# Kernel tuning notes

Measured on AMD Instinct MI355X. Metric: run time of the kernel, lower is better.

Reference implementation:

```python
import jax, jax.numpy as jnp
import numpy as np

B, N, H, E, OBS, A, AFF, EFF = 2, 50000, 64, 1_000_000, 128, 18, 512, 256


def setup_inputs() -> dict:
    key = jax.random.key(0)
    ks = jax.random.split(key, 20)
    s = 0.05  # small init to keep gates/tanh unsaturated
    return {
        "obs": jax.random.normal(ks[0], (B, OBS), jnp.float32),
        "state": jax.random.normal(ks[1], (B, N, H), jnp.float32) * 0.1,
        "W_in": jax.random.normal(ks[2], (OBS, H), jnp.float32) * s,
        "b_in": jnp.zeros((H,), jnp.float32),
        "W_msg": jax.random.normal(ks[3], (H, H), jnp.float32) * s,
        "W_gate": jax.random.normal(ks[4], (2 * H, H), jnp.float32) * s,
        "b_gate": jnp.zeros((H,), jnp.float32),
        "W_cand": jax.random.normal(ks[5], (2 * H, H), jnp.float32) * s,
        "b_cand": jnp.zeros((H,), jnp.float32),
        "W_dec": jax.random.normal(ks[6], (H, H), jnp.float32) * s,
        "b_dec": jnp.zeros((H,), jnp.float32),
        "W_mean": jax.random.normal(ks[7], (H, A), jnp.float32) * s,
        "b_mean": jnp.zeros((A,), jnp.float32),
        "W_ls": jax.random.normal(ks[8], (H, A), jnp.float32) * s,
        "b_ls": jnp.zeros((A,), jnp.float32),
        "src_index": jax.random.randint(ks[9], (E,), 0, N),
        "dst_index": jax.random.randint(ks[10], (E,), 0, N),
        "afferent_idx": jax.random.randint(ks[11], (AFF,), 0, N),
        "efferent_idx": jax.random.randint(ks[12], (EFF,), 0, N),
    }


def reference(obs, state, W_in, b_in, W_msg, W_gate, b_gate, W_cand, b_cand,
              W_dec, b_dec, W_mean, b_mean, W_ls, b_ls,
              src_index, dst_index, afferent_idx, efferent_idx):
    # inject obs projection into afferent node slots
    projected = obs @ W_in + b_in                                   # [B, H]
    injected = jnp.zeros_like(state).at[:, afferent_idx, :].set(projected[:, None, :])
    # gather-project-scatter message passing over the edge list
    src_msgs = state[:, src_index, :] @ W_msg                       # [B, E, H]
    messages = jnp.zeros_like(state).at[:, dst_index, :].add(src_msgs)
    # GRU-style gated update
    combined = messages + injected
    gate_in = jnp.concatenate([state, combined], axis=-1)           # [B, N, 2H]
    z = jax.nn.sigmoid(gate_in @ W_gate + b_gate)
    cand = jnp.tanh(gate_in @ W_cand + b_cand)
    next_state = (1.0 - z) * state + z * cand
    # mean-pool readout over efferent nodes, then policy heads
    readout = next_state[:, efferent_idx, :].mean(axis=1)           # [B, H]
    decoded = jnp.tanh(readout @ W_dec + b_dec)
    mean = decoded @ W_mean + b_mean
    log_std = jnp.clip(decoded @ W_ls + b_ls, -5.0, 2.0)
    return mean, log_std, next_state
```

## Files before the change

### kernel.cpp

```cpp
#include <hip/hip_runtime.h>
#include <hip/hip_bf16.h>

constexpr int kN   = 50000;
constexpr int kH   = 64;
constexpr int kB   = 2;
constexpr int kE   = 1000000;
constexpr int kObs = 128;
constexpr int kA   = 18;
constexpr int kAff = 512;
constexpr int kEff = 256;
constexpr int kNH  = kN * kH;
constexpr int kOutOff = 2 * kB * kA;
constexpr int kRanges = 8;
constexpr int kNr  = kN / kRanges;
constexpr int kChunks = 64;
constexpr int kEc  = kE / kChunks;
constexpr int kHistB = kRanges * kChunks;
constexpr int kPackPerR = (kNr + 127) / 128;
constexpr int kPackBlocks = kRanges * kPackPerR;
constexpr int kWprepBlocks = 20;
constexpr int kScanB = (kN + 255) / 256;
constexpr int kGatB = kRanges * 1563;
constexpr int kUpdPerR = (kNr + 31) / 32;
constexpr int kUpdB = kRanges * kUpdPerR;

typedef __attribute__((ext_vector_type(8))) short short8_t;
typedef __attribute__((ext_vector_type(4))) float f32x4_t;

__device__ __forceinline__ float ldf(const void* p, int i, int f32) {
  if (f32) return ((const float*)p)[i];
  unsigned short u = ((const unsigned short*)p)[i];
  union { unsigned int x; float f; } v; v.x = ((unsigned int)u) << 16; return v.f;
}
__device__ __forceinline__ void stf(void* p, int i, float val, int f32) {
  if (f32) ((float*)p)[i] = val;
  else ((__hip_bfloat16*)p)[i] = __float2bfloat16(val);
}
__device__ __forceinline__ float lo16(unsigned int w) {
  union { unsigned int i; float f; } v; v.i = w << 16; return v.f;
}
__device__ __forceinline__ float hi16(unsigned int w) {
  union { unsigned int i; float f; } v; v.i = w & 0xffff0000u; return v.f;
}
__device__ __forceinline__ float b2f(unsigned short u) {
  union { unsigned int i; float f; } v; v.i = ((unsigned int)u) << 16; return v.f;
}
__device__ __forceinline__ unsigned int f2b(float f) {
  union { float f; unsigned int u; } v; v.f = f;
  unsigned int r = v.u + 0x7fffu + ((v.u >> 16) & 1u);
  return r >> 16;
}
__device__ __forceinline__ float fsig(float x) {
  return __builtin_amdgcn_rcpf(1.f + __expf(-x));
}
__device__ __forceinline__ float ftanh(float x) {
  return 1.f - 2.f * __builtin_amdgcn_rcpf(__expf(2.f * x) + 1.f);
}
__device__ __forceinline__ int detect64(const unsigned short* wprobe, int t) {
  int hits = 0;
  for (int k = 0; k < 4; ++k) {
    unsigned short u = wprobe[(t * 4 + k) * 2];
    int e = (u >> 7) & 0xFF;
    if ((u & 0x7FFFu) != 0 && e >= 108 && e <= 128) hits++;
  }
  for (int off = 32; off; off >>= 1) hits += __shfl_down(hits, off);
  return (hits < 128) ? 1 : 0;
}

extern "C" __global__ __launch_bounds__(1024) void k_prep(
    const unsigned short* __restrict__ wprobe,
    const void* __restrict__ obs,
    const void* __restrict__ W_in,
    const void* __restrict__ b_in,
    const int* __restrict__ aff_idx,
    const int* __restrict__ dst,
    const void* __restrict__ W_msg,
    const void* __restrict__ W_gate,
    const void* __restrict__ W_cand,
    int* __restrict__ dflag,
    int* __restrict__ flags,
    float* __restrict__ projected,
    int* __restrict__ deg_c,
    unsigned short* __restrict__ wt,
    float* __restrict__ eff_acc) {
  __shared__ int sdeg[kNr];
  int t = threadIdx.x, b = blockIdx.x;
  if (b == 0) {
    __shared__ int sflag;
    if (t < 64) { int f = detect64(wprobe, t); if (t == 0) { sflag = f; dflag[0] = f; } }
    for (int i = t; i < kN; i += 1024) flags[i] = 0;
    if (t < 128) eff_acc[t] = 0.f;
    __syncthreads();
    int f32 = sflag;
    if (t < kAff) flags[aff_idx[t]] = 1;
    if (t < kB * kH) {
      int bb = t >> 6, h = t & 63;
      float acc = ldf(b_in, h, f32);
      for (int o = 0; o < kObs; ++o)
        acc += ldf(obs, bb * kObs + o, f32) * ldf(W_in, o * kH + h, f32);
      projected[t] = acc;
    }
  } else if (b <= kHistB) {
    int h = b - 1, r = h & 7, c = h >> 3;
    int r0 = r * kNr;
    for (int i = t; i < kNr; i += 1024) sdeg[i] = 0;
    __syncthreads();
    int end = (c + 1) * kEc;
    for (int e = c * kEc + t; e < end; e += 1024) {
      unsigned rel = (unsigned)(dst[e] - r0);
      if (rel < (unsigned)kNr) atomicAdd(&sdeg[rel], 1);
    }
    __syncthreads();
    for (int i = t; i < kNr; i += 1024) deg_c[c * kN + r0 + i] = sdeg[i];
  } else {
    __shared__ int sflag;
    if (t < 64) { int f = detect64(wprobe, t); if (t == 0) sflag = f; }
    __syncthreads();
    int f32 = sflag;
    int i = (b - 1 - kHistB) * 1024 + t;
    if (i < 4096) {
      int n = i >> 6, k = i & 63;
      wt[i] = (unsigned short)f2b(ldf(W_msg, k * 64 + n, f32));
    } else if (i < 12288) {
      int j = i - 4096; int n = j >> 7, k = j & 127;
      wt[i] = (unsigned short)f2b(ldf(W_gate, k * 64 + n, f32));
    } else if (i < 20480) {
      int j = i - 12288; int n = j >> 7, k = j & 127;
      wt[i] = (unsigned short)f2b(ldf(W_cand, k * 64 + n, f32));
    }
  }
}

extern "C" __global__ void k_scan1(const int* __restrict__ deg_c,
                                   int* __restrict__ row_off,
                                   int* __restrict__ partials) {
  __shared__ int sd[256];
  int t = threadIdx.x;
  int n = blockIdx.x * 256 + t;
  int s = 0;
  if (n < kN) {
    for (int c = 0; c < kChunks; ++c) s += deg_c[c * kN + n];
  }
  sd[t] = s;
  __syncthreads();
  for (int off = 1; off < 256; off <<= 1) {
    int v = (t >= off) ? sd[t - off] : 0;
    __syncthreads();
    sd[t] += v;
    __syncthreads();
  }
  int excl = sd[t] - s;
  if (t == 255) partials[blockIdx.x] = sd[255];
  if (n < kN) row_off[n] = excl;
}

extern "C" __global__ void k_scan3(int* __restrict__ row_off,
                                   const int* __restrict__ partials,
                                   int* __restrict__ deg_c) {
  __shared__ int sd[256];
  int t = threadIdx.x;
  int s = 0;
  for (int j = t; j < (int)blockIdx.x; j += 256) s += partials[j];
  sd[t] = s;
  __syncthreads();
  for (int off = 128; off; off >>= 1) {
    if (t < off) sd[t] += sd[t + off];
    __syncthreads();
  }
  int base = sd[0];
  int n = blockIdx.x * 256 + t;
  if (n < kN) {
    int v = row_off[n] + base;
    row_off[n] = v;
    int run = v;
#pragma unroll 8
    for (int c = 0; c < kChunks; ++c) {
      int d = deg_c[c * kN + n];
      deg_c[c * kN + n] = run;
      run += d;
    }
  }
  if (blockIdx.x == 0 && t == 0) row_off[kN] = kE;
}

extern "C" __global__ __launch_bounds__(1024) void k_scatter(
    const int* __restrict__ src,
    const int* __restrict__ dst,
    const int* __restrict__ chunk_base,
    int* __restrict__ sorted_src,
    const unsigned short* __restrict__ wprobe,
    const void* __restrict__ state,
    unsigned int* __restrict__ pack) {
  __shared__ int scur[kNr];
  int t = threadIdx.x;
  if (blockIdx.x < kHistB) {
    int r = blockIdx.x & 7, c = blockIdx.x >> 3;
    int r0 = r * kNr;
    for (int i = t; i < kNr; i += 1024) scur[i] = chunk_base[c * kN + r0 + i];
    __syncthreads();
    int end = (c + 1) * kEc;
    for (int e = c * kEc + t; e < end; e += 1024) {
      unsigned rel = (unsigned)(dst[e] - r0);
      if (rel < (unsigned)kNr) {
        int pos = atomicAdd(&scur[rel], 1);
        sorted_src[pos] = src[e];
      }
    }
  } else {
    __shared__ int sflag;
    if (t < 64) { int f = detect64(wprobe, t); if (t == 0) sflag = f; }
    __syncthreads();
    int f32 = sflag;
    int p = blockIdx.x - kHistB;
    int x = p & 7, j = p >> 3;
    int nb = x * kNr + j * 128;
    int nl = min(nb + 128, (x + 1) * kNr);
    int i = nb * 64 + t * 8;
    if (i < nl * 64) {
      uint4 o0, o1;
      if (!f32) {
        uint4 a = *(const uint4*)((const unsigned short*)state + i);
        uint4 c4 = *(const uint4*)((const unsigned short*)state + kNH + i);
        o0.x = (a.x & 0xffffu) | (c4.x << 16);
        o0.y = (a.x >> 16)     | (c4.x & 0xffff0000u);
        o0.z = (a.y & 0xffffu) | (c4.y << 16);
        o0.w = (a.y >> 16)     | (c4.y & 0xffff0000u);
        o1.x = (a.z & 0xffffu) | (c4.z << 16);
        o1.y = (a.z >> 16)     | (c4.z & 0xffff0000u);
        o1.z = (a.w & 0xffffu) | (c4.w << 16);
        o1.w = (a.w >> 16)     | (c4.w & 0xffff0000u);
      } else {
        const float* sf = (const float*)state;
        unsigned int w[8];
#pragma unroll
        for (int k = 0; k < 8; ++k)
          w[k] = f2b(sf[i + k]) | (f2b(sf[kNH + i + k]) << 16);
        o0 = make_uint4(w[0], w[1], w[2], w[3]);
        o1 = make_uint4(w[4], w[5], w[6], w[7]);
      }
      *(uint4*)&pack[i] = o0;
      *(uint4*)&pack[i + 4] = o1;
    }
  }
}

extern "C" __global__ __launch_bounds__(256) void k_gather(
    const unsigned int* __restrict__ pack,
    const int* __restrict__ row_off,
    const int* __restrict__ sorted_src,
    unsigned int* __restrict__ agg) {
  int wave = threadIdx.x >> 6, lane = threadIdx.x & 63;
  int x = blockIdx.x & 7, j = blockIdx.x >> 3;
  int local = j * 4 + wave;
  if (local >= kNr) return;
  int n = x * kNr + local;
  int s  = row_off[n];
  int en = row_off[n + 1];
  int g = lane >> 4, col = lane & 15;
  const uint4* pk4 = (const uint4*)pack;
  float a0x = 0.f, a0y = 0.f, a0z = 0.f, a0w = 0.f;
  float a1x = 0.f, a1y = 0.f, a1z = 0.f, a1w = 0.f;
  for (int e = s; e < en; e += 8) {
#pragma unroll
    for (int h = 0; h < 2; ++h) {
      int ee = e + h * 4 + g;
      int idx = sorted_src[min(ee, en - 1)];
      uint4 wv = pk4[idx * 16 + col];
      if (ee >= en) { wv.x = 0u; wv.y = 0u; wv.z = 0u; wv.w = 0u; }
      a0x += lo16(wv.x); a1x += hi16(wv.x);
      a0y += lo16(wv.y); a1y += hi16(wv.y);
      a0z += lo16(wv.z); a1z += hi16(wv.z);
      a0w += lo16(wv.w); a1w += hi16(wv.w);
    }
  }
  a0x += __shfl_xor(a0x, 16); a0x += __shfl_xor(a0x, 32);
  a0y += __shfl_xor(a0y, 16); a0y += __shfl_xor(a0y, 32);
  a0z += __shfl_xor(a0z, 16); a0z += __shfl_xor(a0z, 32);
  a0w += __shfl_xor(a0w, 16); a0w += __shfl_xor(a0w, 32);
  a1x += __shfl_xor(a1x, 16); a1x += __shfl_xor(a1x, 32);
  a1y += __shfl_xor(a1y, 16); a1y += __shfl_xor(a1y, 32);
  a1z += __shfl_xor(a1z, 16); a1z += __shfl_xor(a1z, 32);
  a1w += __shfl_xor(a1w, 16); a1w += __shfl_xor(a1w, 32);
  if (g == 0) {
    uint4 o;
    o.x = f2b(a0x) | (f2b(a1x) << 16);
    o.y = f2b(a0y) | (f2b(a1y) << 16);
    o.z = f2b(a0z) | (f2b(a1z) << 16);
    o.w = f2b(a0w) | (f2b(a1w) << 16);
    ((uint4*)agg)[n * 16 + col] = o;
  }
}

extern "C" __global__ __launch_bounds__(256) void k_update(
    const unsigned int* __restrict__ pk,
    const unsigned short* __restrict__ wt,
    const void* __restrict__ b_gate,
    const void* __restrict__ b_cand,
    const unsigned int* __restrict__ agg,
    const int* __restrict__ flags,
    const float* __restrict__ projected,
    const int* __restrict__ dflag,
    void* __restrict__ out,
    const int* __restrict__ eff_idx,
    float* __restrict__ eff_acc) {
  __shared__ uint4 lx4[1088];
  __shared__ int smatch[256];
  __shared__ int smcnt;
  unsigned short* lx = (unsigned short*)lx4;
  int f32 = dflag[0];
  int t = threadIdx.x;
  int w = t >> 6, lane = t & 63;
  int q = lane >> 4, l15 = lane & 15;
  int rowb = w * 16;
  int x = blockIdx.x & 7, jb = blockIdx.x >> 3;
  int nd0 = x * kNr + jb * 32;
  int rend = (x + 1) * kNr;
  if (nd0 >= rend) return;
  int ndw = nd0 + w * 8;
  if (t == 0) smcnt = 0;

  const uint4* pk4 = (const uint4*)pk;
  const uint4* ag4 = (const uint4*)agg;
  for (int j = lane; j < 128; j += 64) {
    int ndl = j >> 4, c4 = j & 15;
    int ndg = min(ndw + ndl, rend - 1);
    uint4 pv = pk4[ndg * 16 + c4];
    uint4 av = ag4[ndg * 16 + c4];
    int r0 = rowb + 2 * ndl;
    *(uint2*)&lx[r0 * 136 + c4 * 4] =
        make_uint2((pv.x & 0xffffu) | (pv.y << 16), (pv.z & 0xffffu) | (pv.w << 16));
    *(uint2*)&lx[(r0 + 1) * 136 + c4 * 4] =
        make_uint2((pv.x >> 16) | (pv.y & 0xffff0000u), (pv.z >> 16) | (pv.w & 0xffff0000u));
    *(uint2*)&lx[r0 * 136 + 64 + c4 * 4] =
        make_uint2((av.x & 0xffffu) | (av.y << 16), (av.z & 0xffffu) | (av.w << 16));
    *(uint2*)&lx[(r0 + 1) * 136 + 64 + c4 * 4] =
        make_uint2((av.x >> 16) | (av.y & 0xffff0000u), (av.z >> 16) | (av.w & 0xffff0000u));
  }

  const unsigned short* wm = wt;
  const unsigned short* wg = wt + 4096;
  const unsigned short* wc = wt + 12288;

  short8_t a0 = *(const short8_t*)&lx[(rowb + l15) * 136 + 64 + q * 8];
  short8_t a1 = *(const short8_t*)&lx[(rowb + l15) * 136 + 96 + q * 8];
  f32x4_t msgc[4];
#pragma unroll
  for (int ct = 0; ct < 4; ++ct) {
    f32x4_t acc = {0.f, 0.f, 0.f, 0.f};
    short8_t b0 = *(const short8_t*)&wm[(ct * 16 + l15) * 64 + q * 8];
    short8_t b1 = *(const short8_t*)&wm[(ct * 16 + l15) * 64 + 32 + q * 8];
    acc = __builtin_amdgcn_mfma_f32_16x16x32_bf16(a0, b0, acc, 0, 0, 0);
    acc = __builtin_amdgcn_mfma_f32_16x16x32_bf16(a1, b1, acc, 0, 0, 0);
    msgc[ct] = acc;
  }
  int nA = ndw + q * 2, nB = nA + 1;
  int flA = (nA < rend) ? flags[nA] : 0;
  int flB = (nB < rend) ? flags[nB] : 0;
#pragma unroll
  for (int ct = 0; ct < 4; ++ct) {
    int col = ct * 16 + l15;
    float pj0 = projected[col], pj1 = projected[64 + col];
#pragma unroll
    for (int r = 0; r < 4; ++r) {
      int row = rowb + q * 4 + r;
      int fl = (r < 2) ? flA : flB;
      float inj = fl ? ((row & 1) ? pj1 : pj0) : 0.f;
      lx[row * 136 + 64 + col] = (unsigned short)f2b(msgc[ct][r] + inj);
    }
  }

  short8_t xa[4];
#pragma unroll
  for (int ks = 0; ks < 4; ++ks)
    xa[ks] = *(const short8_t*)&lx[(rowb + l15) * 136 + ks * 32 + q * 8];
  float ps[16];
#pragma unroll
  for (int ct = 0; ct < 4; ++ct)
#pragma unroll
    for (int rp = 0; rp < 2; ++rp) {
      int row = rowb + q * 4 + 2 * rp;
      ps[ct * 4 + rp * 2 + 0] = b2f(lx[row * 136 + ct * 16 + l15]);
      ps[ct * 4 + rp * 2 + 1] = b2f(lx[(row + 1) * 136 + ct * 16 + l15]);
    }
  float* soutw = (float*)((char*)lx4 + w * 4352);
#pragma unroll
  for (int ct = 0; ct < 4; ++ct) {
    f32x4_t accg = {0.f, 0.f, 0.f, 0.f}, accc = {0.f, 0.f, 0.f, 0.f};
#pragma unroll
    for (int ks = 0; ks < 4; ++ks) {
      short8_t bg = *(const short8_t*)&wg[(ct * 16 + l15) * 128 + ks * 32 + q * 8];
      short8_t bc = *(const short8_t*)&wc[(ct * 16 + l15) * 128 + ks * 32 + q * 8];
      accg = __builtin_amdgcn_mfma_f32_16x16x32_bf16(xa[ks], bg, accg, 0, 0, 0);
      accc = __builtin_amdgcn_mfma_f32_16x16x32_bf16(xa[ks], bc, accc, 0, 0, 0);
    }
    int col = ct * 16 + l15;
    float bgv = ldf(b_gate, col, f32), bcv = ldf(b_cand, col, f32);
#pragma unroll
    for (int rp = 0; rp < 2; ++rp) {
      int r = q * 4 + 2 * rp;
      float z0 = fsig(accg[2 * rp] + bgv);
      float c0 = ftanh(accc[2 * rp] + bcv);
      soutw[r * 64 + col] = (1.f - z0) * ps[ct * 4 + rp * 2 + 0] + z0 * c0;
      float z1 = fsig(accg[2 * rp + 1] + bgv);
      float c1 = ftanh(accc[2 * rp + 1] + bcv);
      soutw[(r + 1) * 64 + col] = (1.f - z1) * ps[ct * 4 + rp * 2 + 1] + z1 * c1;
    }
  }
  __syncthreads();

  int nlim = min(32, rend - nd0);
  if (t < kEff) {
    unsigned rel = (unsigned)(eff_idx[t] - nd0);
    if (rel < (unsigned)nlim) { int s = atomicAdd(&smcnt, 1); smatch[s] = (int)rel; }
  }
  __syncthreads();

  int nvalid = nlim * 64;
  if (f32) {
    float* po = (float*)out + kOutOff;
#pragma unroll
    for (int p = 0; p < 2; ++p)
      for (int j = t * 4; j < nvalid; j += 1024) {
        int ndl = j >> 6, c = j & 63;
        int wv = ndl >> 3, r = ((ndl & 7) << 1) + p;
        float4 v = *(float4*)((char*)lx4 + wv * 4352 + r * 256 + c * 4);
        *(float4*)(po + p * kNH + nd0 * 64 + j) = v;
      }
  } else {
    unsigned short* po = (unsigned short*)out + kOutOff;
#pragma unroll
    for (int p = 0; p < 2; ++p)
      for (int j = t * 8; j < nvalid; j += 2048) {
        int ndl = j >> 6, c = j & 63;
        int wv = ndl >> 3, r = ((ndl & 7) << 1) + p;
        const char* base = (const char*)lx4 + wv * 4352 + r * 256 + c * 4;
        float4 v0 = *(const float4*)base;
        float4 v1 = *(const float4*)(base + 16);
        uint4 o;
        o.x = f2b(v0.x) | (f2b(v0.y) << 16);
        o.y = f2b(v0.z) | (f2b(v0.w) << 16);
        o.z = f2b(v1.x) | (f2b(v1.y) << 16);
        o.w = f2b(v1.z) | (f2b(v1.w) << 16);
        *(uint4*)(po + p * kNH + nd0 * 64 + j) = o;
      }
  }

  int cnt = smcnt;
  for (int m = 0; m < cnt; ++m) {
    int rel = smatch[m];
    if (t < 128) {
      int p = t >> 6, c = t & 63;
      int wv = rel >> 3, r = ((rel & 7) << 1) + p;
      float v = *(const float*)((const char*)lx4 + wv * 4352 + r * 256 + c * 4);
      if (!f32) v = b2f((unsigned short)f2b(v));
      atomicAdd(&eff_acc[p * 64 + c], v);
    }
  }
}

extern "C" __global__ void k_readout(const void* __restrict__ W_dec,
                                     const void* __restrict__ b_dec,
                                     const void* __restrict__ W_mean,
                                     const void* __restrict__ b_mean,
                                     const void* __restrict__ W_ls,
                                     const void* __restrict__ b_ls,
                                     const float* __restrict__ eff_acc,
                                     const int* __restrict__ dflag,
                                     void* __restrict__ out) {
  __shared__ float ro[128], dec[128];
  int f32 = dflag[0];
  int t = threadIdx.x;
  if (t < 128) ro[t] = eff_acc[t] * (1.f / kEff);
  __syncthreads();
  if (t < 128) {
    int bb = t >> 6, h = t & 63;
    float d = ldf(b_dec, h, f32);
    for (int k = 0; k < 64; ++k) d += ro[bb * 64 + k] * ldf(W_dec, k * 64 + h, f32);
    dec[t] = tanhf(d);
  }
  __syncthreads();
  if (t < kB * kA) {
    int bb = t / kA, a = t % kA;
    float m = ldf(b_mean, a, f32), l = ldf(b_ls, a, f32);
    for (int k = 0; k < 64; ++k) {
      float dv = dec[bb * 64 + k];
      m += dv * ldf(W_mean, k * kA + a, f32);
      l += dv * ldf(W_ls, k * kA + a, f32);
    }
    l = fminf(fmaxf(l, -5.f), 2.f);
    stf(out, t, m, f32);
    stf(out, kB * kA + t, l, f32);
  }
}

extern "C" void kernel_launch(void* const* d_in, const int* in_sizes, int n_in,
                              void* d_out, int out_size, void* d_ws, size_t ws_size,
                              hipStream_t stream) {
  (void)in_sizes; (void)n_in; (void)out_size; (void)ws_size;
  const void* obs    = d_in[0];
  const void* state  = d_in[1];
  const void* W_in   = d_in[2];
  const void* b_in   = d_in[3];
  const void* W_msg  = d_in[4];
  const void* W_gate = d_in[5];
  const void* b_gate = d_in[6];
  const void* W_cand = d_in[7];
  const void* b_cand = d_in[8];
  const void* W_dec  = d_in[9];
  const void* b_dec  = d_in[10];
  const void* W_mean = d_in[11];
  const void* b_mean = d_in[12];
  const void* W_ls   = d_in[13];
  const void* b_ls   = d_in[14];
  const int* src = (const int*)d_in[15];
  const int* dst = (const int*)d_in[16];
  const int* aff = (const int*)d_in[17];
  const int* eff = (const int*)d_in[18];

  int* wsp        = (int*)d_ws;
  int* flags      = wsp;
  int* deg_c      = flags + kN;
  int* row_off    = deg_c + kChunks * kN;
  int* partials   = row_off + (kN + 64);
  int* dflag      = partials + 512;
  float* projected = (float*)(dflag + 16);
  float* eff_acc   = projected + 128;
  int* sorted_src  = (int*)(eff_acc + 128);
  unsigned int* pk  = (unsigned int*)(sorted_src + kE);
  unsigned int* agg = pk + kNH;
  unsigned short* wt = (unsigned short*)(agg + kNH);

  k_prep<<<1 + kHistB + kWprepBlocks, 1024, 0, stream>>>(
      (const unsigned short*)W_cand, obs, W_in, b_in, aff, dst,
      W_msg, W_gate, W_cand, dflag, flags, projected, deg_c, wt, eff_acc);
  k_scan1<<<kScanB, 256, 0, stream>>>(deg_c, row_off, partials);
  k_scan3<<<kScanB, 256, 0, stream>>>(row_off, partials, deg_c);
  k_scatter<<<kHistB + kPackBlocks, 1024, 0, stream>>>(
      src, dst, deg_c, sorted_src, (const unsigned short*)W_cand, state, pk);
  k_gather<<<kGatB, 256, 0, stream>>>(pk, row_off, sorted_src, agg);
  k_update<<<kUpdB, 256, 0, stream>>>(pk, wt, b_gate, b_cand,
                                      agg, flags, projected, dflag, d_out,
                                      eff, eff_acc);
  k_readout<<<1, 128, 0, stream>>>(W_dec, b_dec, W_mean, b_mean, W_ls, b_ls,
                                   eff_acc, dflag, d_out);
}
```

Baseline: 257.4 us.

## Shrink update kernel to one wave per block and privatize efferent readout sums

```diff
diff --git a/kernel.cpp b/kernel.cpp
--- a/kernel.cpp
+++ b/kernel.cpp
@@ -21,7 +21,7 @@
 constexpr int kWprepBlocks = 20;
 constexpr int kScanB = (kN + 255) / 256;
 constexpr int kGatB = kRanges * 1563;
-constexpr int kUpdPerR = (kNr + 31) / 32;
+constexpr int kUpdPerR = (kNr + 7) / 8;
 constexpr int kUpdB = kRanges * kUpdPerR;
 
 typedef __attribute__((ext_vector_type(8))) short short8_t;
@@ -89,7 +89,7 @@
     __shared__ int sflag;
     if (t < 64) { int f = detect64(wprobe, t); if (t == 0) { sflag = f; dflag[0] = f; } }
     for (int i = t; i < kN; i += 1024) flags[i] = 0;
-    if (t < 128) eff_acc[t] = 0.f;
+    eff_acc[t] = 0.f;
     __syncthreads();
     int f32 = sflag;
     if (t < kAff) flags[aff_idx[t]] = 1;
@@ -291,7 +291,7 @@
   }
 }
 
-extern "C" __global__ __launch_bounds__(256) void k_update(
+extern "C" __global__ __launch_bounds__(64, 6) void k_update(
     const unsigned int* __restrict__ pk,
     const unsigned short* __restrict__ wt,
     const void* __restrict__ b_gate,
@@ -303,21 +303,18 @@
     void* __restrict__ out,
     const int* __restrict__ eff_idx,
     float* __restrict__ eff_acc) {
-  __shared__ uint4 lx4[1088];
+  __shared__ uint4 lx4[274];
   __shared__ int smatch[256];
   __shared__ int smcnt;
   unsigned short* lx = (unsigned short*)lx4;
   int f32 = dflag[0];
-  int t = threadIdx.x;
-  int w = t >> 6, lane = t & 63;
+  int lane = threadIdx.x;
   int q = lane >> 4, l15 = lane & 15;
-  int rowb = w * 16;
   int x = blockIdx.x & 7, jb = blockIdx.x >> 3;
-  int nd0 = x * kNr + jb * 32;
+  int ndw = x * kNr + jb * 8;
   int rend = (x + 1) * kNr;
-  if (nd0 >= rend) return;
-  int ndw = nd0 + w * 8;
-  if (t == 0) smcnt = 0;
+  if (ndw >= rend) return;
+  if (lane == 0) smcnt = 0;
 
   const uint4* pk4 = (const uint4*)pk;
   const uint4* ag4 = (const uint4*)agg;
@@ -326,7 +323,7 @@
     int ndg = min(ndw + ndl, rend - 1);
     uint4 pv = pk4[ndg * 16 + c4];
     uint4 av = ag4[ndg * 16 + c4];
-    int r0 = rowb + 2 * ndl;
+    int r0 = 2 * ndl;
     *(uint2*)&lx[r0 * 136 + c4 * 4] =
         make_uint2((pv.x & 0xffffu) | (pv.y << 16), (pv.z & 0xffffu) | (pv.w << 16));
     *(uint2*)&lx[(r0 + 1) * 136 + c4 * 4] =
@@ -336,13 +333,14 @@
     *(uint2*)&lx[(r0 + 1) * 136 + 64 + c4 * 4] =
         make_uint2((av.x >> 16) | (av.y & 0xffff0000u), (av.z >> 16) | (av.w & 0xffff0000u));
   }
+  __syncthreads();
 
   const unsigned short* wm = wt;
   const unsigned short* wg = wt + 4096;
   const unsigned short* wc = wt + 12288;
 
-  short8_t a0 = *(const short8_t*)&lx[(rowb + l15) * 136 + 64 + q * 8];
-  short8_t a1 = *(const short8_t*)&lx[(rowb + l15) * 136 + 96 + q * 8];
+  short8_t a0 = *(const short8_t*)&lx[l15 * 136 + 64 + q * 8];
+  short8_t a1 = *(const short8_t*)&lx[l15 * 136 + 96 + q * 8];
   f32x4_t msgc[4];
 #pragma unroll
   for (int ct = 0; ct < 4; ++ct) {
@@ -362,7 +360,7 @@
     float pj0 = projected[col], pj1 = projected[64 + col];
 #pragma unroll
     for (int r = 0; r < 4; ++r) {
-      int row = rowb + q * 4 + r;
+      int row = q * 4 + r;
       int fl = (r < 2) ? flA : flB;
       float inj = fl ? ((row & 1) ? pj1 : pj0) : 0.f;
       lx[row * 136 + 64 + col] = (unsigned short)f2b(msgc[ct][r] + inj);
@@ -372,17 +370,17 @@
   short8_t xa[4];
 #pragma unroll
   for (int ks = 0; ks < 4; ++ks)
-    xa[ks] = *(const short8_t*)&lx[(rowb + l15) * 136 + ks * 32 + q * 8];
+    xa[ks] = *(const short8_t*)&lx[l15 * 136 + ks * 32 + q * 8];
   float ps[16];
 #pragma unroll
   for (int ct = 0; ct < 4; ++ct)
 #pragma unroll
     for (int rp = 0; rp < 2; ++rp) {
-      int row = rowb + q * 4 + 2 * rp;
+      int row = q * 4 + 2 * rp;
       ps[ct * 4 + rp * 2 + 0] = b2f(lx[row * 136 + ct * 16 + l15]);
       ps[ct * 4 + rp * 2 + 1] = b2f(lx[(row + 1) * 136 + ct * 16 + l15]);
     }
-  float* soutw = (float*)((char*)lx4 + w * 4352);
+  float* soutw = (float*)lx4;
 #pragma unroll
   for (int ct = 0; ct < 4; ++ct) {
     f32x4_t accg = {0.f, 0.f, 0.f, 0.f}, accc = {0.f, 0.f, 0.f, 0.f};
@@ -408,9 +406,9 @@
   }
   __syncthreads();
 
-  int nlim = min(32, rend - nd0);
-  if (t < kEff) {
-    unsigned rel = (unsigned)(eff_idx[t] - nd0);
+  int nlim = min(8, rend - ndw);
+  for (int i = lane; i < kEff; i += 64) {
+    unsigned rel = (unsigned)(eff_idx[i] - ndw);
     if (rel < (unsigned)nlim) { int s = atomicAdd(&smcnt, 1); smatch[s] = (int)rel; }
   }
   __syncthreads();
@@ -420,20 +418,18 @@
     float* po = (float*)out + kOutOff;
 #pragma unroll
     for (int p = 0; p < 2; ++p)
-      for (int j = t * 4; j < nvalid; j += 1024) {
+      for (int j = lane * 4; j < nvalid; j += 256) {
         int ndl = j >> 6, c = j & 63;
-        int wv = ndl >> 3, r = ((ndl & 7) << 1) + p;
-        float4 v = *(float4*)((char*)lx4 + wv * 4352 + r * 256 + c * 4);
-        *(float4*)(po + p * kNH + nd0 * 64 + j) = v;
+        float4 v = *(float4*)((char*)lx4 + ((ndl * 2 + p) * 64 + c) * 4);
+        *(float4*)(po + p * kNH + ndw * 64 + j) = v;
       }
   } else {
     unsigned short* po = (unsigned short*)out + kOutOff;
 #pragma unroll
     for (int p = 0; p < 2; ++p)
-      for (int j = t * 8; j < nvalid; j += 2048) {
+      for (int j = lane * 8; j < nvalid; j += 512) {
         int ndl = j >> 6, c = j & 63;
-        int wv = ndl >> 3, r = ((ndl & 7) << 1) + p;
-        const char* base = (const char*)lx4 + wv * 4352 + r * 256 + c * 4;
+        const char* base = (const char*)lx4 + ((ndl * 2 + p) * 64 + c) * 4;
         float4 v0 = *(const float4*)base;
         float4 v1 = *(const float4*)(base + 16);
         uint4 o;
@@ -441,20 +437,23 @@
         o.y = f2b(v0.z) | (f2b(v0.w) << 16);
         o.z = f2b(v1.x) | (f2b(v1.y) << 16);
         o.w = f2b(v1.z) | (f2b(v1.w) << 16);
-        *(uint4*)(po + p * kNH + nd0 * 64 + j) = o;
+        *(uint4*)(po + p * kNH + ndw * 64 + j) = o;
       }
   }
 
   int cnt = smcnt;
-  for (int m = 0; m < cnt; ++m) {
-    int rel = smatch[m];
-    if (t < 128) {
-      int p = t >> 6, c = t & 63;
-      int wv = rel >> 3, r = ((rel & 7) << 1) + p;
-      float v = *(const float*)((const char*)lx4 + wv * 4352 + r * 256 + c * 4);
-      if (!f32) v = b2f((unsigned short)f2b(v));
-      atomicAdd(&eff_acc[p * 64 + c], v);
-    }
+  if (cnt) {
+    float a0s = 0.f, a1s = 0.f;
+    const float* sf = (const float*)lx4;
+    for (int m = 0; m < cnt; ++m) {
+      int rel = smatch[m];
+      float v0 = sf[(rel * 2 + 0) * 64 + lane];
+      float v1 = sf[(rel * 2 + 1) * 64 + lane];
+      if (!f32) { v0 = b2f((unsigned short)f2b(v0)); v1 = b2f((unsigned short)f2b(v1)); }
+      a0s += v0; a1s += v1;
+    }
+    atomicAdd(&eff_acc[x * 128 + lane], a0s);
+    atomicAdd(&eff_acc[x * 128 + 64 + lane], a1s);
   }
 }
 
@@ -470,7 +469,12 @@
   __shared__ float ro[128], dec[128];
   int f32 = dflag[0];
   int t = threadIdx.x;
-  if (t < 128) ro[t] = eff_acc[t] * (1.f / kEff);
+  if (t < 128) {
+    float s = 0.f;
+#pragma unroll
+    for (int r = 0; r < kRanges; ++r) s += eff_acc[r * 128 + t];
+    ro[t] = s * (1.f / kEff);
+  }
   __syncthreads();
   if (t < 128) {
     int bb = t >> 6, h = t & 63;
@@ -525,7 +529,7 @@
   int* dflag      = partials + 512;
   float* projected = (float*)(dflag + 16);
   float* eff_acc   = projected + 128;
-  int* sorted_src  = (int*)(eff_acc + 128);
+  int* sorted_src  = (int*)(eff_acc + 1024);
   unsigned int* pk  = (unsigned int*)(sorted_src + kE);
   unsigned int* agg = pk + kNH;
   unsigned short* wt = (unsigned short*)(agg + kNH);
@@ -538,9 +542,9 @@
   k_scatter<<<kHistB + kPackBlocks, 1024, 0, stream>>>(
       src, dst, deg_c, sorted_src, (const unsigned short*)W_cand, state, pk);
   k_gather<<<kGatB, 256, 0, stream>>>(pk, row_off, sorted_src, agg);
-  k_update<<<kUpdB, 256, 0, stream>>>(pk, wt, b_gate, b_cand,
-                                      agg, flags, projected, dflag, d_out,
-                                      eff, eff_acc);
+  k_update<<<kUpdB, 64, 0, stream>>>(pk, wt, b_gate, b_cand,
+                                     agg, flags, projected, dflag, d_out,
+                                     eff, eff_acc);
   k_readout<<<1, 128, 0, stream>>>(W_dec, b_dec, W_mean, b_mean, W_ls, b_ls,
                                    eff_acc, dflag, d_out);
 }
```

Measured after the change: 271.1 us. +5.3%, slower.
